# Optimization experiments

Hardware: AMD Instinct MI355X
Metric: run time of the kernel (lower is better)

The kernel has to match this reference:

```python
import jax, jax.numpy as jnp
import numpy as np

HID = 2048
H = 16
D_NOPE = 128
D_ROPE = 64
HEAD_DIM = D_NOPE + D_ROPE  # 192
V_DIM = 128
KV_RANK = 512
Q_RANK = 1536
THETA = 10000.0
EPS = 1e-6
B, S = 2, 2048


def _rope_cos_sin(seq_len):
    # half-dim frequencies: cos/sin have shape (seq_len, D_ROPE//2)
    inv_freq = 1.0 / (THETA ** (jnp.arange(0, D_ROPE, 2, dtype=jnp.float32) / D_ROPE))
    freqs = jnp.arange(seq_len, dtype=jnp.float32)[:, None] * inv_freq[None, :]
    return jnp.cos(freqs), jnp.sin(freqs)


def _apply_rope(x, cos, sin):
    # x: (..., D_ROPE); cos/sin broadcastable to (..., D_ROPE//2)
    half = x.shape[-1] // 2
    x1, x2 = x[..., :half], x[..., half:]
    return jnp.concatenate([x1 * cos - x2 * sin, x2 * cos + x1 * sin], axis=-1)


def _rmsnorm(x, w):
    ms = jnp.mean(jnp.square(x), axis=-1, keepdims=True)
    return x * jax.lax.rsqrt(ms + EPS) * w


def setup_inputs() -> dict:
    key = jax.random.key(0)
    ks = jax.random.split(key, 7)
    std = 0.02
    return {
        "x": jax.random.normal(ks[0], (B, S, HID), dtype=jnp.float32),
        "w_q_down": jax.random.normal(ks[1], (HID, Q_RANK), dtype=jnp.float32) * std,
        "w_q_up": jax.random.normal(ks[2], (Q_RANK, H * HEAD_DIM), dtype=jnp.float32) * std,
        "w_kv_down": jax.random.normal(ks[3], (HID, KV_RANK + D_ROPE), dtype=jnp.float32) * std,
        "kv_norm_w": jnp.ones((KV_RANK,), dtype=jnp.float32),
        "w_kv_up": jax.random.normal(ks[4], (KV_RANK, H * (D_NOPE + V_DIM)), dtype=jnp.float32) * std,
        "w_out": jax.random.normal(ks[5], (H * V_DIM, HID), dtype=jnp.float32) * std,
    }


def reference(x, w_q_down, w_q_up, w_kv_down, kv_norm_w, w_kv_up, w_out):
    b, s, _ = x.shape
    scale = 1.0 / np.sqrt(HEAD_DIM)

    # query: low-rank down then up, split into nope/rope parts
    q = (x @ w_q_down) @ w_q_up                      # (b, s, H*HEAD_DIM)
    q = q.reshape(b, s, H, HEAD_DIM)
    q_nope, q_rope = q[..., :D_NOPE], q[..., D_NOPE:]

    # KV: compressed latent + rope key component
    kv_full = x @ w_kv_down                          # (b, s, KV_RANK + D_ROPE)
    kv_c, k_rope = kv_full[..., :KV_RANK], kv_full[..., KV_RANK:]
    kv_c = _rmsnorm(kv_c, kv_norm_w)

    kv_exp = (kv_c @ w_kv_up).reshape(b, s, H, D_NOPE + V_DIM)
    k_nope, v = kv_exp[..., :D_NOPE], kv_exp[..., D_NOPE:]

    # RoPE (no past_kv -> q_offset = 0, kv_len = s)
    cos, sin = _rope_cos_sin(s)                      # (s, D_ROPE//2)
    cos4, sin4 = cos[None, :, None, :], sin[None, :, None, :]
    q_rope = _apply_rope(q_rope, cos4, sin4)         # (b, s, H, D_ROPE)
    k_rope = _apply_rope(k_rope, cos[None], sin[None])  # (b, s, D_ROPE)

    k_rope_h = jnp.broadcast_to(k_rope[:, :, None, :], (b, s, H, D_ROPE))
    k = jnp.concatenate([k_nope, k_rope_h], axis=-1)     # (b, s, H, HEAD_DIM)
    q_full = jnp.concatenate([q_nope, q_rope], axis=-1)  # (b, s, H, HEAD_DIM)

    # causal SDPA
    scores = jnp.einsum("bqhd,bkhd->bhqk", q_full, k) * scale
    causal = jnp.tril(jnp.ones((s, s), dtype=bool))
    scores = jnp.where(causal[None, None], scores, jnp.finfo(scores.dtype).min)
    attn = jax.nn.softmax(scores, axis=-1)
    out = jnp.einsum("bhqk,bkhd->bqhd", attn, v)     # (b, s, H, V_DIM)
    out = out.reshape(b, s, H * V_DIM)
    return out @ w_out
```

## Files before the change

kernel.cpp:

```cpp
#include <hip/hip_runtime.h>
#include <hip/hip_bf16.h>
#include <math.h>

#define HID    2048
#define NH     16
#define D_NOPE 128
#define D_ROPE 64
#define HD     192
#define V_DIM  128
#define KV_RANK 512
#define Q_RANK  1536
#define BATCH  2
#define SEQ    2048
#define ROWS   (BATCH*SEQ)

typedef __attribute__((ext_vector_type(8))) short short8;
typedef __attribute__((ext_vector_type(4))) float f32x4;

__device__ __forceinline__ unsigned short f2bf(float x) {
    unsigned int u = __float_as_uint(x);
    unsigned int r = (u + 0x7fffu + ((u >> 16) & 1u)) >> 16;
    return (unsigned short)r;
}
__device__ __forceinline__ float bf2f(unsigned short u) {
    return __uint_as_float((unsigned int)u << 16);
}

typedef const __attribute__((address_space(1))) unsigned int gu32;
typedef __attribute__((address_space(3))) unsigned int lu32;
__device__ __forceinline__ void gl_lds16(const void* g, void* l) {
    __builtin_amdgcn_global_load_lds((gu32*)g, (lu32*)l, 16, 0, 0);
}

template<int CTRL>
__device__ __forceinline__ float dpp_mv(float x) {
    return __int_as_float(__builtin_amdgcn_update_dpp(
        __float_as_int(x), __float_as_int(x), CTRL, 0xF, 0xF, true));
}
__device__ __forceinline__ float rowmax16(float x) {
    x = fmaxf(x, dpp_mv<0xB1>(x));
    x = fmaxf(x, dpp_mv<0x4E>(x));
    x = fmaxf(x, dpp_mv<0x141>(x));
    x = fmaxf(x, dpp_mv<0x140>(x));
    return x;
}

__global__ void rope_table_kernel(float* __restrict__ table) {
    int idx = blockIdx.x * 256 + threadIdx.x;
    int pos = idx >> 6, u = idx & 63;
    int i = u & 31;
    float invf = expf((float)i * (-9.210340371976184f / 32.0f));
    float ang = (float)pos * invf;
    table[idx] = (u < 32) ? cosf(ang) : sinf(ang);
}

__global__ __launch_bounds__(256) void convert_bf16_kernel(
    const float* __restrict__ src, unsigned short* __restrict__ dst)
{
    size_t i = (size_t)(blockIdx.x * 256 + threadIdx.x) * 4;
    float4 v = *(const float4*)(src + i);
    ushort4 u;
    u.x = f2bf(v.x); u.y = f2bf(v.y); u.z = f2bf(v.z); u.w = f2bf(v.w);
    *(ushort4*)(dst + i) = u;
}

__global__ __launch_bounds__(256) void transpose_bf16_kernel(
    const float* __restrict__ src, unsigned short* __restrict__ dst, int K, int N)
{
    __shared__ float T[64][65];
    const int n0 = blockIdx.x * 64, k0 = blockIdx.y * 64;
    const int t = threadIdx.x;
    const int c4 = t & 15, r = t >> 4;
    #pragma unroll
    for (int i = 0; i < 4; i++) {
        int row = r + i * 16;
        float4 v = *(const float4*)(src + (size_t)(k0 + row) * N + n0 + c4 * 4);
        T[row][c4*4+0] = v.x; T[row][c4*4+1] = v.y;
        T[row][c4*4+2] = v.z; T[row][c4*4+3] = v.w;
    }
    __syncthreads();
    #pragma unroll
    for (int i = 0; i < 4; i++) {
        int nrow = r + i * 16;
        ushort4 u;
        u.x = f2bf(T[c4*4+0][nrow]); u.y = f2bf(T[c4*4+1][nrow]);
        u.z = f2bf(T[c4*4+2][nrow]); u.w = f2bf(T[c4*4+3][nrow]);
        *(ushort4*)(dst + (size_t)(n0 + nrow) * K + k0 + c4 * 4) = u;
    }
}

template<int BN, bool OUT_BF16>
__global__ __launch_bounds__(256) void bgemm_kernel(
    const unsigned short* __restrict__ A,
    const unsigned short* __restrict__ Bt,
    void* __restrict__ Cv,
    int M, int N, int K)
{
    constexpr int NT = BN / 32;
    constexpr int NSLAB = 8 + BN / 16;
    const int tid  = threadIdx.x;
    const int w    = tid >> 6;
    const int lane = tid & 63;
    const int n16  = lane & 15, quad = lane >> 4;
    const int m0 = blockIdx.y * 128;
    const int n0 = blockIdx.x * BN;
    const int moff = (w & 1) * 64;
    const int noff = (w >> 1) * (NT * 16);

    __shared__ unsigned short As[128 * 32];
    __shared__ unsigned short Bs[BN * 32];

    const unsigned short* gp[4];
    unsigned short* lp[4];
    int ns = 0;
    const int rl = lane >> 2, sc = lane & 3;
    for (int s = w; s < NSLAB; s += 4) {
        int kc = sc ^ (((s * 16 + rl) >> 1) & 3);
        if (s < 8) {
            gp[ns] = A + (size_t)(m0 + s * 16 + rl) * K + kc * 8;
            lp[ns] = As + s * 512;
        } else {
            int sb = s - 8;
            gp[ns] = Bt + (size_t)(n0 + sb * 16 + rl) * K + kc * 8;
            lp[ns] = Bs + sb * 512;
        }
        ns++;
    }

    const int swz = (quad ^ ((n16 >> 1) & 3)) * 8;
    int aoff[4], boff[NT];
    #pragma unroll
    for (int mt = 0; mt < 4; mt++) aoff[mt] = (moff + mt * 16 + n16) * 32 + swz;
    #pragma unroll
    for (int nt = 0; nt < NT; nt++) boff[nt] = (noff + nt * 16 + n16) * 32 + swz;

    f32x4 acc[4][NT];
    #pragma unroll
    for (int mt = 0; mt < 4; mt++)
        #pragma unroll
        for (int nt = 0; nt < NT; nt++) acc[mt][nt] = (f32x4){0.f, 0.f, 0.f, 0.f};

    for (int k0 = 0; k0 < K; k0 += 32) {
        #pragma unroll
        for (int j = 0; j < 4; j++) if (j < ns) gl_lds16(gp[j], lp[j]);
        #pragma unroll
        for (int j = 0; j < 4; j++) if (j < ns) gp[j] += 32;
        __syncthreads();

        short8 af[4], bfr[NT];
        #pragma unroll
        for (int mt = 0; mt < 4; mt++) af[mt] = *(const short8*)(As + aoff[mt]);
        #pragma unroll
        for (int nt = 0; nt < NT; nt++) bfr[nt] = *(const short8*)(Bs + boff[nt]);
        #pragma unroll
        for (int mt = 0; mt < 4; mt++)
            #pragma unroll
            for (int nt = 0; nt < NT; nt++)
                acc[mt][nt] = __builtin_amdgcn_mfma_f32_16x16x32_bf16(
                    af[mt], bfr[nt], acc[mt][nt], 0, 0, 0);
        __syncthreads();
    }

    #pragma unroll
    for (int mt = 0; mt < 4; mt++)
        #pragma unroll
        for (int nt = 0; nt < NT; nt++)
            #pragma unroll
            for (int r = 0; r < 4; r++) {
                size_t idx = (size_t)(m0 + moff + mt * 16 + quad * 4 + r) * N
                           + n0 + noff + nt * 16 + n16;
                if (OUT_BF16) ((unsigned short*)Cv)[idx] = f2bf(acc[mt][nt][r]);
                else          ((float*)Cv)[idx] = acc[mt][nt][r];
            }
}

__global__ __launch_bounds__(256) void kv_norm_rope_kernel(
    const float* __restrict__ kv_full,
    const float* __restrict__ w,
    const float* __restrict__ table,
    unsigned short* __restrict__ kv_cb,
    unsigned short* __restrict__ k_rope_b)
{
    const int row = blockIdx.x;
    const int tid = threadIdx.x;
    const float* src = kv_full + (size_t)row * 576;
    float v0 = src[tid], v1 = src[tid + 256];
    float ss = v0*v0 + v1*v1;
    #pragma unroll
    for (int off = 32; off > 0; off >>= 1) ss += __shfl_down(ss, off);
    __shared__ float red[4];
    __shared__ float msh;
    if ((tid & 63) == 0) red[tid >> 6] = ss;
    __syncthreads();
    if (tid == 0) msh = (red[0] + red[1] + red[2] + red[3]) * (1.0f / 512.0f);
    __syncthreads();
    float f = rsqrtf(msh + 1e-6f);
    kv_cb[(size_t)row * 512 + tid]       = f2bf(v0 * f * w[tid]);
    kv_cb[(size_t)row * 512 + tid + 256] = f2bf(v1 * f * w[tid + 256]);
    if (tid < 32) {
        int pos = row & (SEQ - 1);
        float c = table[pos*64 + tid], s = table[pos*64 + 32 + tid];
        float x1 = src[512 + tid], x2 = src[512 + 32 + tid];
        k_rope_b[(size_t)row * 64 + tid]      = f2bf(x1*c - x2*s);
        k_rope_b[(size_t)row * 64 + 32 + tid] = f2bf(x2*c + x1*s);
    }
}

__global__ __launch_bounds__(256) void q_rope_b_kernel(
    unsigned short* __restrict__ qb16, const float* __restrict__ table)
{
    int g = blockIdx.x * 8 + (threadIdx.x >> 5);
    int i = threadIdx.x & 31;
    int row = g >> 4, h = g & 15;
    size_t base = (size_t)row * (NH*HD) + h * HD + D_NOPE;
    int pos = row & (SEQ - 1);
    float c = table[pos*64 + i], s = table[pos*64 + 32 + i];
    float x1 = bf2f(qb16[base + i]), x2 = bf2f(qb16[base + 32 + i]);
    qb16[base + i]      = f2bf(x1*c - x2*s);
    qb16[base + 32 + i] = f2bf(x2*c + x1*s);
}

__global__ __launch_bounds__(256) void pack_vt_kernel(
    const unsigned short* __restrict__ kv_exp_b, unsigned short* __restrict__ Vmat)
{
    const int st = blockIdx.x;
    const int h  = blockIdx.y;
    const int b  = blockIdx.z;
    const int tid = threadIdx.x;
    const int s0 = st * 64;
    __shared__ float T[64][129];

    #pragma unroll
    for (int t = 0; t < 8; t++) {
        int idx = tid + t * 256;
        int tokr = idx >> 5, c4 = idx & 31;
        ushort4 u = *(const ushort4*)(kv_exp_b +
            ((size_t)(b*SEQ) + s0 + tokr) * 4096 + h*256 + 128 + c4*4);
        T[tokr][c4*4+0] = bf2f(u.x); T[tokr][c4*4+1] = bf2f(u.y);
        T[tokr][c4*4+2] = bf2f(u.z); T[tokr][c4*4+3] = bf2f(u.w);
    }
    __syncthreads();

    int d = tid >> 1, sh = (tid & 1) * 32;
    unsigned short* op = Vmat + ((size_t)((b*NH + h) * V_DIM + d)) * SEQ + s0 + sh;
    #pragma unroll
    for (int j = 0; j < 32; j += 2) {
        ushort2 u;
        u.x = f2bf(T[sh + j][d]);
        u.y = f2bf(T[sh + j + 1][d]);
        *(ushort2*)(op + j) = u;
    }
}

__global__ __launch_bounds__(256, 3) void flash_mfma_kernel(
    const unsigned short* __restrict__ qb16,
    const unsigned short* __restrict__ kv_exp_b,
    const unsigned short* __restrict__ k_rope_b,
    const unsigned short* __restrict__ Vmat,
    unsigned short* __restrict__ attnb)
{
    const int bid  = blockIdx.x;
    const int xcd  = bid & 7, slot = bid >> 3;
    const int grp  = xcd + 8 * (slot >> 5);
    const int qb   = 31 - (slot & 31);
    const int h    = grp & 15, b = grp >> 4;
    const int tid  = threadIdx.x;
    const int w    = tid >> 6;
    const int lane = tid & 63;
    const int n16  = lane & 15;
    const int quad = lane >> 4;

    const int q0 = qb * 64 + w * 16;
    const char* kNopeB = (const char*)(kv_exp_b + (size_t)b * SEQ * 4096 + h * 256);
    const char* kRopeB = (const char*)(k_rope_b + (size_t)b * SEQ * 64);
    const char* vByte  = (const char*)(Vmat + (size_t)(b*NH + h) * V_DIM * SEQ);

    __shared__ unsigned short Ks[2][6144];
    __shared__ unsigned short Vs[2][4096];
    __shared__ unsigned short Plds[4][16][40];

    const char* gK[2]; int lK[2];
    #pragma unroll
    for (int t = 0; t < 2; t++) {
        int idx = t * 256 + tid;
        int kc = idx >> 7, key = (idx >> 2) & 31, sc = idx & 3;
        int scs = sc ^ ((key >> 1) & 3);
        gK[t] = kNopeB + (size_t)key * 8192 + kc * 64 + scs * 16;
        lK[t] = idx * 16;
    }
    const char* gR; int lR;
    {
        int kc = tid >> 7, key = (tid >> 2) & 31, sc = tid & 3;
        int scs = sc ^ ((key >> 1) & 3);
        gR = kRopeB + (size_t)key * 128 + kc * 64 + scs * 16;
        lR = (512 + tid) * 16;
    }
    const char* gV[2]; int lV[2];
    #pragma unroll
    for (int t = 0; t < 2; t++) {
        int idx = t * 256 + tid;
        int d = idx >> 2, sc = idx & 3;
        int scs = sc ^ ((d >> 1) & 3);
        gV[t] = vByte + (size_t)d * (SEQ * 2) + scs * 16;
        lV[t] = idx * 16;
    }

    auto stage = [&](int kt, int bufsel) {
        const size_t koff = (size_t)kt * 32;
        #pragma unroll
        for (int t = 0; t < 2; t++)
            gl_lds16(gK[t] + koff * 8192, (char*)Ks[bufsel] + lK[t]);
        gl_lds16(gR + koff * 128, (char*)Ks[bufsel] + lR);
        #pragma unroll
        for (int t = 0; t < 2; t++)
            gl_lds16(gV[t] + koff * 2, (char*)Vs[bufsel] + lV[t]);
    };

    short8 qf[6];
    {
        const unsigned short* qp = qb16 + ((size_t)(b*SEQ) + q0 + n16) * (NH*HD)
                                 + h * HD + quad * 8;
        #pragma unroll
        for (int kc = 0; kc < 6; kc++)
            qf[kc] = *(const short8*)(qp + kc * 32);
    }

    short8 onesf;
    #pragma unroll
    for (int j = 0; j < 8; j++) onesf[j] = (short)0x3F80;

    f32x4 O[9];
    #pragma unroll
    for (int c = 0; c < 9; c++) O[c] = (f32x4){0.f, 0.f, 0.f, 0.f};
    float mrow[4] = {-INFINITY, -INFINITY, -INFINITY, -INFINITY};

    const float scale = 0.07216878364870322f;
    const int swz = (quad ^ ((n16 >> 1) & 3)) * 8;
    const int ntB = 2 * qb + 2;

    stage(0, 0);
    int cur = 0;
    for (int kt = 0; kt < ntB; kt++) {
        __syncthreads();
        if (kt + 1 < ntB) stage(kt + 1, cur ^ 1);
        const int k0 = kt * 32;

        if (k0 <= q0 + 15) {
            const unsigned short* KsB = Ks[cur];
            const unsigned short* VsB = Vs[cur];

            f32x4 S[2];
            __builtin_amdgcn_s_setprio(1);
            #pragma unroll
            for (int half = 0; half < 2; half++) {
                f32x4 acc = (f32x4){0.f, 0.f, 0.f, 0.f};
                const int keyoff = (half * 16 + n16) * 32 + swz;
                #pragma unroll
                for (int kc = 0; kc < 6; kc++) {
                    short8 kf = *(const short8*)(KsB + kc * 1024 + keyoff);
                    acc = __builtin_amdgcn_mfma_f32_16x16x32_bf16(qf[kc], kf, acc, 0, 0, 0);
                }
                S[half] = acc;
            }
            __builtin_amdgcn_s_setprio(0);

            float p0[4], p1[4], tmax[4];
            float growth = -INFINITY;
            #pragma unroll
            for (int r = 0; r < 4; r++) {
                int row = q0 + quad*4 + r;
                float s0v = (k0 + n16      <= row) ? S[0][r] * scale : -INFINITY;
                float s1v = (k0 + 16 + n16 <= row) ? S[1][r] * scale : -INFINITY;
                p0[r] = s0v; p1[r] = s1v;
                tmax[r] = rowmax16(fmaxf(s0v, s1v));
                growth = fmaxf(growth, tmax[r] - mrow[r]);
            }
            if (!__all(growth <= 6.0f)) {
                #pragma unroll
                for (int r = 0; r < 4; r++) {
                    float mnew = fmaxf(mrow[r], tmax[r]);
                    float alpha = __expf(mrow[r] - mnew);
                    mrow[r] = mnew;
                    #pragma unroll
                    for (int c = 0; c < 9; c++) O[c][r] *= alpha;
                }
            }
            #pragma unroll
            for (int r = 0; r < 4; r++) {
                float e0 = __expf(p0[r] - mrow[r]);
                float e1 = __expf(p1[r] - mrow[r]);
                unsigned short* pw = &Plds[w][quad*4 + r][0];
                pw[n16]      = f2bf(e0);
                pw[16 + n16] = f2bf(e1);
            }

            short8 pf = *(const short8*)(&Plds[w][n16][quad * 8]);
            __builtin_amdgcn_s_setprio(1);
            #pragma unroll
            for (int c = 0; c < 8; c++) {
                short8 vf = *(const short8*)(VsB + (c * 16 + n16) * 32 + swz);
                O[c] = __builtin_amdgcn_mfma_f32_16x16x32_bf16(pf, vf, O[c], 0, 0, 0);
            }
            O[8] = __builtin_amdgcn_mfma_f32_16x16x32_bf16(pf, onesf, O[8], 0, 0, 0);
            __builtin_amdgcn_s_setprio(0);
        }
        cur ^= 1;
    }

    float invl[4];
    #pragma unroll
    for (int r = 0; r < 4; r++) invl[r] = 1.0f / O[8][r];
    #pragma unroll
    for (int c = 0; c < 8; c++) {
        #pragma unroll
        for (int r = 0; r < 4; r++) {
            size_t tok = (size_t)b * SEQ + q0 + quad*4 + r;
            attnb[tok * (NH*V_DIM) + h * V_DIM + c*16 + n16] = f2bf(O[c][r] * invl[r]);
        }
    }
}

extern "C" void kernel_launch(void* const* d_in, const int* in_sizes, int n_in,
                              void* d_out, int out_size, void* d_ws, size_t ws_size,
                              hipStream_t stream)
{
    const float* x         = (const float*)d_in[0];
    const float* w_q_down  = (const float*)d_in[1];
    const float* w_q_up    = (const float*)d_in[2];
    const float* w_kv_down = (const float*)d_in[3];
    const float* kv_norm_w = (const float*)d_in[4];
    const float* w_kv_up   = (const float*)d_in[5];
    const float* w_out     = (const float*)d_in[6];
    float* out = (float*)d_out;
    float* ws  = (float*)d_ws;

    float*          table    = ws;
    unsigned short* xb       = (unsigned short*)(ws + 131072);
    unsigned short* qdb      = (unsigned short*)(ws + 4325376);
    unsigned short* qb16     = (unsigned short*)(ws + 7471104);
    float*          kv_full  = ws + 13762560;
    unsigned short* kv_cb    = (unsigned short*)(ws + 16121856);
    unsigned short* k_rope_b = (unsigned short*)(ws + 17170432);
    unsigned short* kv_exp_b = (unsigned short*)(ws + 17301504);
    unsigned short* Vmat     = (unsigned short*)(ws + 25690112);
    unsigned short* attnb    = (unsigned short*)(ws + 29884416);
    unsigned short* wt1      = (unsigned short*)(ws + 34078720);
    unsigned short* wt2      = (unsigned short*)(ws + 35651584);
    unsigned short* wt3      = (unsigned short*)(ws + 38010880);
    unsigned short* wt4      = (unsigned short*)(ws + 38600704);
    unsigned short* wt5      = (unsigned short*)(ws + 39649280);

    rope_table_kernel<<<512, 256, 0, stream>>>(table);

    convert_bf16_kernel<<<ROWS*HID/1024, 256, 0, stream>>>(x, xb);
    transpose_bf16_kernel<<<dim3(1536/64, 2048/64), 256, 0, stream>>>(w_q_down, wt1, 2048, 1536);
    transpose_bf16_kernel<<<dim3(3072/64, 1536/64), 256, 0, stream>>>(w_q_up,   wt2, 1536, 3072);
    transpose_bf16_kernel<<<dim3(576/64,  2048/64), 256, 0, stream>>>(w_kv_down,wt3, 2048, 576);
    transpose_bf16_kernel<<<dim3(4096/64,  512/64), 256, 0, stream>>>(w_kv_up,  wt4, 512, 4096);
    transpose_bf16_kernel<<<dim3(2048/64, 2048/64), 256, 0, stream>>>(w_out,    wt5, 2048, 2048);

    bgemm_kernel<128, true><<<dim3(1536/128, ROWS/128), 256, 0, stream>>>(xb,  wt1, qdb,  ROWS, 1536, 2048);
    bgemm_kernel<128, true><<<dim3(3072/128, ROWS/128), 256, 0, stream>>>(qdb, wt2, qb16, ROWS, 3072, 1536);
    q_rope_b_kernel<<<8192, 256, 0, stream>>>(qb16, table);

    bgemm_kernel<64, false><<<dim3(576/64, ROWS/128), 256, 0, stream>>>(xb, wt3, kv_full, ROWS, 576, 2048);
    kv_norm_rope_kernel<<<ROWS, 256, 0, stream>>>(kv_full, kv_norm_w, table, kv_cb, k_rope_b);
    bgemm_kernel<128, true><<<dim3(4096/128, ROWS/128), 256, 0, stream>>>(kv_cb, wt4, kv_exp_b, ROWS, 4096, 512);
    pack_vt_kernel<<<dim3(SEQ/64, NH, BATCH), 256, 0, stream>>>(kv_exp_b, Vmat);

    flash_mfma_kernel<<<dim3(1024), 256, 0, stream>>>(qb16, kv_exp_b, k_rope_b, Vmat, attnb);

    bgemm_kernel<128, false><<<dim3(2048/128, ROWS/128), 256, 0, stream>>>(attnb, wt5, out, ROWS, 2048, 2048);
}
```

Measured before the change: 489.7 us.

## Remap GEMM blocks across XCDs and fold softmax scale into exp2

GEMM launches switch to a 1D grid and remap block IDs so that consecutive tiles land on the same XCD (block id mod 8), aiming for better L2 reuse of A/B tiles. The flash kernel drops the per-element scale multiply and computes exp2 with scale*log2e folded into one constant, adjusting the rescale threshold to raw score units. The causal mask is evaluated only on diagonal tiles. The remap assumes the grid size is divisible by 8.

```diff
diff --git a/kernel.cpp b/kernel.cpp
--- a/kernel.cpp
+++ b/kernel.cpp
@@ -102,8 +102,13 @@
     const int w    = tid >> 6;
     const int lane = tid & 63;
     const int n16  = lane & 15, quad = lane >> 4;
-    const int m0 = blockIdx.y * 128;
-    const int n0 = blockIdx.x * BN;
+
+    const int nb   = gridDim.x;
+    const int T8   = nb >> 3;
+    const int nbid = (blockIdx.x & 7) * T8 + (blockIdx.x >> 3);
+    const int gx   = N / BN;
+    const int m0 = (nbid / gx) * 128;
+    const int n0 = (nbid % gx) * BN;
     const int moff = (w & 1) * 64;
     const int noff = (w >> 1) * (NT * 16);
 
@@ -334,7 +339,8 @@
     for (int c = 0; c < 9; c++) O[c] = (f32x4){0.f, 0.f, 0.f, 0.f};
     float mrow[4] = {-INFINITY, -INFINITY, -INFINITY, -INFINITY};
 
-    const float scale = 0.07216878364870322f;
+    const float SCLOG2 = 0.10412779736150104f;
+    const float THRRAW = 83.14f;
     const int swz = (quad ^ ((n16 >> 1) & 3)) * 8;
     const int ntB = 2 * qb + 2;
 
@@ -364,22 +370,31 @@
             }
             __builtin_amdgcn_s_setprio(0);
 
-            float p0[4], p1[4], tmax[4];
+            float p0[4], p1[4];
+            if (k0 + 32 > q0) {
+                #pragma unroll
+                for (int r = 0; r < 4; r++) {
+                    int row = q0 + quad*4 + r;
+                    p0[r] = (k0 + n16      <= row) ? S[0][r] : -INFINITY;
+                    p1[r] = (k0 + 16 + n16 <= row) ? S[1][r] : -INFINITY;
+                }
+            } else {
+                #pragma unroll
+                for (int r = 0; r < 4; r++) { p0[r] = S[0][r]; p1[r] = S[1][r]; }
+            }
+
+            float tmax[4];
             float growth = -INFINITY;
             #pragma unroll
             for (int r = 0; r < 4; r++) {
-                int row = q0 + quad*4 + r;
-                float s0v = (k0 + n16      <= row) ? S[0][r] * scale : -INFINITY;
-                float s1v = (k0 + 16 + n16 <= row) ? S[1][r] * scale : -INFINITY;
-                p0[r] = s0v; p1[r] = s1v;
-                tmax[r] = rowmax16(fmaxf(s0v, s1v));
+                tmax[r] = rowmax16(fmaxf(p0[r], p1[r]));
                 growth = fmaxf(growth, tmax[r] - mrow[r]);
             }
-            if (!__all(growth <= 6.0f)) {
+            if (!__all(growth <= THRRAW)) {
                 #pragma unroll
                 for (int r = 0; r < 4; r++) {
                     float mnew = fmaxf(mrow[r], tmax[r]);
-                    float alpha = __expf(mrow[r] - mnew);
+                    float alpha = exp2f((mrow[r] - mnew) * SCLOG2);
                     mrow[r] = mnew;
                     #pragma unroll
                     for (int c = 0; c < 9; c++) O[c][r] *= alpha;
@@ -387,8 +402,8 @@
             }
             #pragma unroll
             for (int r = 0; r < 4; r++) {
-                float e0 = __expf(p0[r] - mrow[r]);
-                float e1 = __expf(p1[r] - mrow[r]);
+                float e0 = exp2f((p0[r] - mrow[r]) * SCLOG2);
+                float e1 = exp2f((p1[r] - mrow[r]) * SCLOG2);
                 unsigned short* pw = &Plds[w][quad*4 + r][0];
                 pw[n16]      = f2bf(e0);
                 pw[16 + n16] = f2bf(e1);
@@ -459,16 +474,16 @@
     transpose_bf16_kernel<<<dim3(4096/64,  512/64), 256, 0, stream>>>(w_kv_up,  wt4, 512, 4096);
     transpose_bf16_kernel<<<dim3(2048/64, 2048/64), 256, 0, stream>>>(w_out,    wt5, 2048, 2048);
 
-    bgemm_kernel<128, true><<<dim3(1536/128, ROWS/128), 256, 0, stream>>>(xb,  wt1, qdb,  ROWS, 1536, 2048);
-    bgemm_kernel<128, true><<<dim3(3072/128, ROWS/128), 256, 0, stream>>>(qdb, wt2, qb16, ROWS, 3072, 1536);
+    bgemm_kernel<128, true><<<dim3(384),  256, 0, stream>>>(xb,  wt1, qdb,  ROWS, 1536, 2048);
+    bgemm_kernel<128, true><<<dim3(768),  256, 0, stream>>>(qdb, wt2, qb16, ROWS, 3072, 1536);
     q_rope_b_kernel<<<8192, 256, 0, stream>>>(qb16, table);
 
-    bgemm_kernel<64, false><<<dim3(576/64, ROWS/128), 256, 0, stream>>>(xb, wt3, kv_full, ROWS, 576, 2048);
+    bgemm_kernel<64, false><<<dim3(288),  256, 0, stream>>>(xb, wt3, kv_full, ROWS, 576, 2048);
     kv_norm_rope_kernel<<<ROWS, 256, 0, stream>>>(kv_full, kv_norm_w, table, kv_cb, k_rope_b);
-    bgemm_kernel<128, true><<<dim3(4096/128, ROWS/128), 256, 0, stream>>>(kv_cb, wt4, kv_exp_b, ROWS, 4096, 512);
+    bgemm_kernel<128, true><<<dim3(1024), 256, 0, stream>>>(kv_cb, wt4, kv_exp_b, ROWS, 4096, 512);
     pack_vt_kernel<<<dim3(SEQ/64, NH, BATCH), 256, 0, stream>>>(kv_exp_b, Vmat);
 
     flash_mfma_kernel<<<dim3(1024), 256, 0, stream>>>(qb16, kv_exp_b, k_rope_b, Vmat, attnb);
 
-    bgemm_kernel<128, false><<<dim3(2048/128, ROWS/128), 256, 0, stream>>>(attnb, wt5, out, ROWS, 2048, 2048);
-}
+    bgemm_kernel<128, false><<<dim3(512), 256, 0, stream>>>(attnb, wt5, out, ROWS, 2048, 2048);
+}
```

After: 482.8 us. About the same (-1.4%).
